# Performance work log

Measured on AMD Instinct MI355X. Metric: run time of the kernel, lower is better.

Reference implementation:

```python
import jax, jax.numpy as jnp
import numpy as np
from jax import lax


def _ramp_filter_real(size):
    # torch ramp_filter: spatial-domain ramp, FFT is purely real (even symmetric)
    image_n = np.concatenate([np.arange(1, size // 2 + 1, 2),
                              np.arange(size // 2 - 1, 0, -2)]).astype(np.float64)
    f = np.zeros(size, dtype=np.float64)
    f[0] = 0.25
    f[1::2] = -1.0 / (np.pi * image_n) ** 2
    return (2.0 * np.real(np.fft.fft(f))).astype(np.float32)  # [size]


def setup_inputs() -> dict:
    key = jax.random.key(0)
    # sinogram: [B, C, detector_bins, n_angles]
    x = jax.random.normal(key, (4, 1, 512, 180), dtype=jnp.float32)
    return {"x": x}


def reference(x):
    B, C, S, A = x.shape  # S = in_size = it_size (circle=True), A = n_angles
    # ---- ramp filtering along detector axis (axis=2) ----
    pad_to = max(64, 1 << int(np.ceil(np.log2(2 * S))))
    xp = jnp.pad(x, ((0, 0), (0, 0), (0, pad_to - S), (0, 0)))
    ramp = jnp.asarray(_ramp_filter_real(pad_to))
    # original multiplies by complex filter r*(1+i); imag part of ifft is 0 for real x,
    # so real part equals standard ramp filtering
    Xf = jnp.fft.fft(xp, axis=2)
    filt = (ramp * (1.0 + 1.0j)).astype(jnp.complex64)
    xfilt = jnp.real(jnp.fft.ifft(Xf * filt[None, None, :, None], axis=2))
    xfilt = xfilt[:, :, :S, :].astype(x.dtype)  # [B,C,S,A]

    # ---- backprojection ----
    unit = jnp.linspace(-1.0, 1.0, S, dtype=x.dtype)
    ygrid, xgrid = jnp.meshgrid(unit, unit, indexing="ij")  # torch.meshgrid 'ij'
    thetas = (jnp.arange(A, dtype=x.dtype) * (np.pi / 180.0)).astype(x.dtype)
    # t coordinate in [-sqrt2, sqrt2]: [A,S,S]
    t = (xgrid[None] * jnp.cos(thetas)[:, None, None]
         - ygrid[None] * jnp.sin(thetas)[:, None, None])
    # grid_sample bilinear, align_corners=True, zeros padding; X coord selects angle i exactly
    p = (t + 1.0) * 0.5 * (S - 1)
    p0 = jnp.floor(p)
    w = (p - p0).astype(x.dtype)
    i0 = p0.astype(jnp.int32)
    i1 = i0 + 1
    v0 = ((i0 >= 0) & (i0 < S)).astype(x.dtype)
    v1 = ((i1 >= 0) & (i1 < S)).astype(x.dtype)
    i0c = jnp.clip(i0, 0, S - 1)
    i1c = jnp.clip(i1, 0, S - 1)

    xa = jnp.moveaxis(xfilt, 3, 0)  # [A,B,C,S]

    def body(acc, inp):
        xa_a, i0a, i1a, wa, v0a, v1a = inp
        g = (xa_a[:, :, i0a] * v0a * (1.0 - wa)
             + xa_a[:, :, i1a] * v1a * wa)  # [B,C,S,S]
        return acc + g, None

    reco0 = jnp.zeros((B, C, S, S), dtype=x.dtype)
    reco, _ = lax.scan(body, reco0, (xa, i0c, i1c, w, v0, v1))

    # circle mask + normalization
    mask = (xgrid ** 2 + ygrid ** 2) <= 1.0
    reco = jnp.where(mask[None, None], reco, 0.0)
    reco = reco * (np.pi / (2.0 * A))
    return reco
```

## Files before the change

### kernel.cpp

```cpp
#include <hip/hip_runtime.h>
#include <math.h>

namespace {

constexpr int BB  = 4;
constexpr int SS  = 512;
constexpr int AA  = 180;
constexpr int PAD = 112;
constexpr int RB  = SS + 2 * PAD;

typedef float v2f __attribute__((ext_vector_type(2)));

__global__ __launch_bounds__(256) void ramp_zero_kernel(
    const float* __restrict__ x, float* __restrict__ xf, float* __restrict__ out) {
  const int t = threadIdx.x;
  {
    const int bid = blockIdx.y * 90 + blockIdx.x;
    float4 z = make_float4(0.f, 0.f, 0.f, 0.f);
    for (int i = bid * 256 + t; i < (BB * SS * SS) / 4; i += 360 * 256)
      ((float4*)out)[i] = z;
  }

  __shared__ __align__(16) float xs[2][2][256];
  __shared__ __align__(16) float G[2][528];
  const int a0 = blockIdx.x * 2;
  const int b  = blockIdx.y;

  const float s  = (float)(M_PI / 360.0);
  const float cc = (float)(-2.0 / (M_PI * M_PI)) * s;
  for (int i = t; i < 528; i += 256) {
    { int kk = i;     float d = (float)(2 * kk - 511); G[0][i] = (kk < 512) ? cc / (d * d) : 0.0f; }
    { int kk = i + 1; float d = (float)(2 * kk - 511); G[1][i] = (kk < 512) ? cc / (d * d) : 0.0f; }
  }

  const float* xb = x + (size_t)b * (SS * AA) + a0;
  {
    int m = t;
    float2 v = *(const float2*)(xb + (size_t)m * AA);
    xs[0][m & 1][m >> 1] = v.x;  xs[1][m & 1][m >> 1] = v.y;
    m = t + 256;
    float2 v2 = *(const float2*)(xb + (size_t)m * AA);
    xs[0][m & 1][m >> 1] = v2.x; xs[1][m & 1][m >> 1] = v2.y;
  }
  __syncthreads();

  const int col = t >> 7;
  const int p   = (t >> 6) & 1;
  const int idx = t & 63;
  const float* Gp = G[p];
  const float* xv = xs[col][1 - p];

  float acc[4] = {0.f, 0.f, 0.f, 0.f};
  float W[8];
  {
    const int A0 = 4 * idx + 252;
    float4 w0 = *(const float4*)(Gp + A0);
    float4 w1 = *(const float4*)(Gp + A0 + 4);
    W[0] = w0.x; W[1] = w0.y; W[2] = w0.z; W[3] = w0.w;
    W[4] = w1.x; W[5] = w1.y; W[6] = w1.z; W[7] = w1.w;
  }

#pragma unroll
  for (int q = 0; q < 64; ++q) {
    const float4 xq = *(const float4*)(xv + 4 * q);
    float4 nw;
    if (q != 63) nw = *(const float4*)(Gp + (4 * idx + 252 - 4 * (q + 1)));
#pragma unroll
    for (int r = 0; r < 4; ++r) {
      acc[r] = fmaf(W[3 + r], xq.x, acc[r]);
      acc[r] = fmaf(W[2 + r], xq.y, acc[r]);
      acc[r] = fmaf(W[1 + r], xq.z, acc[r]);
      acc[r] = fmaf(W[0 + r], xq.w, acc[r]);
    }
    if (q != 63) {
      W[7] = W[3]; W[6] = W[2]; W[5] = W[1]; W[4] = W[0];
      W[0] = nw.x; W[1] = nw.y; W[2] = nw.z; W[3] = nw.w;
    }
  }

  const float selfc = 0.5f * s;
  const float* xsp = xs[col][p];
  float* orow = xf + ((size_t)(b * AA + a0 + col)) * SS;
#pragma unroll
  for (int r = 0; r < 4; ++r)
    orow[p + 8 * idx + 2 * r] = fmaf(selfc, xsp[4 * idx + r], acc[r]);
}

__global__ __launch_bounds__(256, 8) void backproject_kernel(
    const float* __restrict__ xf, float* __restrict__ out) {
  __shared__ __align__(16) v2f P[3][RB];
  __shared__ float2 trig[45];

  const int t     = threadIdx.x;
  const int w     = t >> 6;
  const int lane  = t & 63;
  const int tx    = blockIdx.x;
  const int ty    = blockIdx.y;
  const int b     = blockIdx.z >> 2;
  const int chunk = blockIdx.z & 3;
  const int a0    = chunk * 45;

  {
    const float step = 2.0f / 511.0f;
    float x0 = -1.0f + (float)(tx * 64) * step, x1 = -1.0f + (float)(tx * 64 + 63) * step;
    float y0 = -1.0f + (float)(ty * 16) * step, y1 = -1.0f + (float)(ty * 16 + 15) * step;
    float mx = (x0 <= 0.f && x1 >= 0.f) ? 0.f : fminf(fabsf(x0), fabsf(x1));
    float my = (y0 <= 0.f && y1 >= 0.f) ? 0.f : fminf(fabsf(y0), fabsf(y1));
    if (mx * mx + my * my > 1.0f) return;
  }

  for (int i = t; i < 3 * 2 * PAD; i += 256) {
    int rr = i / 224;
    int o  = i - rr * 224;
    int j  = (o < PAD) ? o : (o + SS);
    P[rr][j] = (v2f){0.f, 0.f};
  }
  if (t < 45) {
    float th = (float)(a0 + t) * (float)(M_PI / 180.0);
    float sn, cn;
    sincosf(th, &sn, &cn);
    trig[t] = make_float2(cn * 255.5f, sn * 255.5f);
  }

  const float* src = xf + ((size_t)b * AA + a0) * SS;

  float2 fw[3], rv[3];
  auto ld = [&](int g) {
    const float* base = src + (size_t)(g * 3) * SS;
#pragma unroll
    for (int k = 0; k < 3; ++k) {
      const float* row = base + k * SS;
      fw[k] = *(const float2*)(row + 2 * t);
      rv[k] = *(const float2*)(row + 510 - 2 * t);
    }
  };
  auto st = [&]() {
#pragma unroll
    for (int k = 0; k < 3; ++k) {
      float4 q = make_float4(fw[k].x, rv[k].y, fw[k].y, rv[k].x);
      *(float4*)&P[k][PAD + 2 * t] = q;
    }
  };

  const int gx = tx * 64 + lane;
  const float step = 2.0f / 511.0f;
  const float xg = __fadd_rn(-1.0f, __fmul_rn((float)gx, step));
  float dy[4];
#pragma unroll
  for (int kk = 0; kk < 4; ++kk) {
    int gy = ty * 16 + w + 4 * kk;
    dy[kk] = -__fadd_rn(-1.0f, __fmul_rn((float)gy, step));
  }

  const float Kp = 255.5f + (float)PAD;
  v2f acc[4];
#pragma unroll
  for (int kk = 0; kk < 4; ++kk) acc[kk] = (v2f){0.f, 0.f};

  ld(0);
  st();
  __syncthreads();

  for (int g = 0; g < 15; ++g) {
    const bool more = (g + 1 < 15);
    if (more) ld(g + 1);
#pragma unroll
    for (int aa = 0; aa < 3; ++aa) {
      const float2 cs = trig[g * 3 + aa];
      const float base = fmaf(xg, cs.x, Kp);
      const v2f* R = P[aa];
#pragma unroll
      for (int kk = 0; kk < 4; ++kk) {
        float p = fmaf(dy[kk], cs.y, base);
        int   I = (int)p;
#if __has_builtin(__builtin_amdgcn_fractf)
        float wq = __builtin_amdgcn_fractf(p);
#else
        float wq = p - floorf(p);
#endif
        struct { v2f a, b; } q;
        __builtin_memcpy(&q, R + I, 16);
        v2f d  = q.b - q.a;
        v2f wv = {wq, wq};
        acc[kk] = (acc[kk] + q.a) + wv * d;
      }
    }
    if (more) {
      __syncthreads();
      st();
      __syncthreads();
    }
  }

  const int gxm  = 511 - gx;
  const float xgm = __fadd_rn(-1.0f, __fmul_rn((float)gxm, step));
  const float xx  = __fmul_rn(xg, xg);
  const float xxm = __fmul_rn(xgm, xgm);
#pragma unroll
  for (int kk = 0; kk < 4; ++kk) {
    int gy  = ty * 16 + w + 4 * kk;
    float yg = -dy[kk];
    float s0 = __fadd_rn(xx, __fmul_rn(yg, yg));
    if (s0 <= 1.0f)
      unsafeAtomicAdd(&out[((size_t)b * SS + gy) * SS + gx], acc[kk].x);
    int gym = 511 - gy;
    float ygm = __fadd_rn(-1.0f, __fmul_rn((float)gym, step));
    float s1 = __fadd_rn(xxm, __fmul_rn(ygm, ygm));
    if (s1 <= 1.0f)
      unsafeAtomicAdd(&out[((size_t)b * SS + gym) * SS + gxm], acc[kk].y);
  }
}

}

extern "C" void kernel_launch(void* const* d_in, const int* in_sizes, int n_in,
                              void* d_out, int out_size, void* d_ws, size_t ws_size,
                              hipStream_t stream) {
  const float* x   = (const float*)d_in[0];
  float*       out = (float*)d_out;
  float*       xf  = (float*)d_ws;

  ramp_zero_kernel<<<dim3(AA / 2, BB), 256, 0, stream>>>(x, xf, out);
  backproject_kernel<<<dim3(4, 32, 16), 256, 0, stream>>>(xf, out);
}
```

Before: 100.4 us.

## Store filtered sinogram as fp16 half2 pairs and stage via async global-to-LDS loads

The ramp kernel now writes the filtered projections as half2 pairs (value and its mirrored counterpart) through a shared-memory staging buffer. The backprojection kernel double-buffers these rows in LDS using global_load_lds direct copies, replacing the register load/store path and one barrier per step. Each bilinear tap now reads 8 bytes instead of 16 and converts half to float. This is meant to cut LDS footprint, global traffic and sync overhead, at the cost of fp16 precision on the filtered data.

```diff
diff --git a/kernel.cpp b/kernel.cpp
--- a/kernel.cpp
+++ b/kernel.cpp
@@ -1,4 +1,5 @@
 #include <hip/hip_runtime.h>
+#include <hip/hip_fp16.h>
 #include <math.h>
 
 namespace {
@@ -7,12 +8,11 @@
 constexpr int SS  = 512;
 constexpr int AA  = 180;
 constexpr int PAD = 112;
-constexpr int RB  = SS + 2 * PAD;
 
 typedef float v2f __attribute__((ext_vector_type(2)));
 
 __global__ __launch_bounds__(256) void ramp_zero_kernel(
-    const float* __restrict__ x, float* __restrict__ xf, float* __restrict__ out) {
+    const float* __restrict__ x, __half2* __restrict__ xf2, float* __restrict__ out) {
   const int t = threadIdx.x;
   {
     const int bid = blockIdx.y * 90 + blockIdx.x;
@@ -23,6 +23,7 @@
 
   __shared__ __align__(16) float xs[2][2][256];
   __shared__ __align__(16) float G[2][528];
+  __shared__ float yb[2][512];
   const int a0 = blockIdx.x * 2;
   const int b  = blockIdx.y;
 
@@ -80,15 +81,24 @@
 
   const float selfc = 0.5f * s;
   const float* xsp = xs[col][p];
-  float* orow = xf + ((size_t)(b * AA + a0 + col)) * SS;
 #pragma unroll
   for (int r = 0; r < 4; ++r)
-    orow[p + 8 * idx + 2 * r] = fmaf(selfc, xsp[4 * idx + r], acc[r]);
+    yb[col][p + 8 * idx + 2 * r] = fmaf(selfc, xsp[4 * idx + r], acc[r]);
+  __syncthreads();
+
+  __half2* orow = xf2 + ((size_t)(b * AA + a0)) * SS;
+#pragma unroll
+  for (int e = 0; e < 2; ++e) {
+    int j = t + e * 256;
+#pragma unroll
+    for (int c2 = 0; c2 < 2; ++c2)
+      orow[c2 * SS + j] = __floats2half2_rn(yb[c2][j], yb[c2][511 - j]);
+  }
 }
 
 __global__ __launch_bounds__(256, 8) void backproject_kernel(
-    const float* __restrict__ xf, float* __restrict__ out) {
-  __shared__ __align__(16) v2f P[3][RB];
+    const __half2* __restrict__ xf2, float* __restrict__ out) {
+  __shared__ __align__(16) __half2 P2[2][3][768];
   __shared__ float2 trig[45];
 
   const int t     = threadIdx.x;
@@ -109,11 +119,14 @@
     if (mx * mx + my * my > 1.0f) return;
   }
 
-  for (int i = t; i < 3 * 2 * PAD; i += 256) {
-    int rr = i / 224;
-    int o  = i - rr * 224;
-    int j  = (o < PAD) ? o : (o + SS);
-    P[rr][j] = (v2f){0.f, 0.f};
+  {
+    const __half2 hz = __floats2half2_rn(0.f, 0.f);
+    for (int i = t; i < 6 * 256; i += 256) {
+      int slot = i >> 8;
+      int o    = i & 255;
+      int j    = (o < PAD) ? o : (o + SS);
+      P2[slot / 3][slot % 3][j] = hz;
+    }
   }
   if (t < 45) {
     float th = (float)(a0 + t) * (float)(M_PI / 180.0);
@@ -122,23 +135,25 @@
     trig[t] = make_float2(cn * 255.5f, sn * 255.5f);
   }
 
-  const float* src = xf + ((size_t)b * AA + a0) * SS;
-
-  float2 fw[3], rv[3];
-  auto ld = [&](int g) {
-    const float* base = src + (size_t)(g * 3) * SS;
-#pragma unroll
-    for (int k = 0; k < 3; ++k) {
-      const float* row = base + k * SS;
-      fw[k] = *(const float2*)(row + 2 * t);
-      rv[k] = *(const float2*)(row + 510 - 2 * t);
-    }
-  };
-  auto st = [&]() {
-#pragma unroll
-    for (int k = 0; k < 3; ++k) {
-      float4 q = make_float4(fw[k].x, rv[k].y, fw[k].y, rv[k].x);
-      *(float4*)&P[k][PAD + 2 * t] = q;
+  const __half2* src = xf2 + ((size_t)b * AA + a0) * SS;
+
+  auto stage = [&](int g, int buf) {
+    const __half2* base = src + (size_t)(g * 3) * SS;
+    {
+      const int sg = w;
+      const __half2* gp = base + (sg >> 1) * SS + (sg & 1) * 256 + lane * 4;
+      void* lp = (void*)&P2[buf][sg >> 1][PAD + (sg & 1) * 256];
+      __builtin_amdgcn_global_load_lds(
+          (const __attribute__((address_space(1))) void*)gp,
+          (__attribute__((address_space(3))) void*)lp, 16, 0, 0);
+    }
+    if (w < 2) {
+      const int sg = 4 + w;
+      const __half2* gp = base + (sg >> 1) * SS + (sg & 1) * 256 + lane * 4;
+      void* lp = (void*)&P2[buf][sg >> 1][PAD + (sg & 1) * 256];
+      __builtin_amdgcn_global_load_lds(
+          (const __attribute__((address_space(1))) void*)gp,
+          (__attribute__((address_space(3))) void*)lp, 16, 0, 0);
     }
   };
 
@@ -157,18 +172,17 @@
 #pragma unroll
   for (int kk = 0; kk < 4; ++kk) acc[kk] = (v2f){0.f, 0.f};
 
-  ld(0);
-  st();
+  stage(0, 0);
   __syncthreads();
 
+  int buf = 0;
   for (int g = 0; g < 15; ++g) {
-    const bool more = (g + 1 < 15);
-    if (more) ld(g + 1);
+    if (g + 1 < 15) stage(g + 1, buf ^ 1);
 #pragma unroll
     for (int aa = 0; aa < 3; ++aa) {
       const float2 cs = trig[g * 3 + aa];
       const float base = fmaf(xg, cs.x, Kp);
-      const v2f* R = P[aa];
+      const __half2* R = P2[buf][aa];
 #pragma unroll
       for (int kk = 0; kk < 4; ++kk) {
         float p = fmaf(dy[kk], cs.y, base);
@@ -178,18 +192,18 @@
 #else
         float wq = p - floorf(p);
 #endif
-        struct { v2f a, b; } q;
-        __builtin_memcpy(&q, R + I, 16);
-        v2f d  = q.b - q.a;
+        struct { __half2 a, b; } q;
+        __builtin_memcpy(&q, R + I, 8);
+        float2 fa = __half22float2(q.a);
+        float2 fb = __half22float2(q.b);
+        v2f av = {fa.x, fa.y};
+        v2f dv = {fb.x - fa.x, fb.y - fa.y};
         v2f wv = {wq, wq};
-        acc[kk] = (acc[kk] + q.a) + wv * d;
+        acc[kk] = (acc[kk] + av) + wv * dv;
       }
     }
-    if (more) {
-      __syncthreads();
-      st();
-      __syncthreads();
-    }
+    __syncthreads();
+    buf ^= 1;
   }
 
   const int gxm  = 511 - gx;
@@ -218,8 +232,8 @@
                               hipStream_t stream) {
   const float* x   = (const float*)d_in[0];
   float*       out = (float*)d_out;
-  float*       xf  = (float*)d_ws;
-
-  ramp_zero_kernel<<<dim3(AA / 2, BB), 256, 0, stream>>>(x, xf, out);
-  backproject_kernel<<<dim3(4, 32, 16), 256, 0, stream>>>(xf, out);
-}
+  __half2*     xf2 = (__half2*)d_ws;
+
+  ramp_zero_kernel<<<dim3(AA / 2, BB), 256, 0, stream>>>(x, xf2, out);
+  backproject_kernel<<<dim3(4, 32, 16), 256, 0, stream>>>(xf2, out);
+}
```

Result: faster. 97.97 us (-2.4%).
